# Performance work log

Hardware: AMD Instinct MI355X
Metric: run time of the kernel (lower is better)

## Reference

```python
import jax, jax.numpy as jnp
import numpy as np

B, DIM, HEADS, H, W, WS, AWS = 8, 64, 4, 256, 256, 8, 8
HD = DIM // HEADS
SCALE = HD ** -0.5


def _grid_sample_zeros(img, grid):
    # img: (N, C, Hi, Wi); grid: (N, Ho, Wo, 2) with (x, y) in [-1, 1]
    # bilinear, align_corners=True, zero padding (matches F.grid_sample)
    N, C, Hi, Wi = img.shape
    gx = (grid[..., 0] + 1.0) * 0.5 * (Wi - 1)
    gy = (grid[..., 1] + 1.0) * 0.5 * (Hi - 1)
    x0 = jnp.floor(gx).astype(jnp.int32); x1 = x0 + 1
    y0 = jnp.floor(gy).astype(jnp.int32); y1 = y0 + 1
    wx1 = gx - x0; wx0 = 1.0 - wx1
    wy1 = gy - y0; wy0 = 1.0 - wy1

    def one(im, x0, x1, y0, y1, wx0, wx1, wy0, wy1):
        def g(yi, xi):
            valid = ((yi >= 0) & (yi < Hi) & (xi >= 0) & (xi < Wi)).astype(im.dtype)
            v = im[:, jnp.clip(yi, 0, Hi - 1), jnp.clip(xi, 0, Wi - 1)]
            return v * valid[None]
        return (g(y0, x0) * (wy0 * wx0)[None] + g(y0, x1) * (wy0 * wx1)[None]
                + g(y1, x0) * (wy1 * wx0)[None] + g(y1, x1) * (wy1 * wx1)[None])

    return jax.vmap(one)(img, x0, x1, y0, y1, wx0, wx1, wy0, wy1)


def _rel_index():
    c = np.stack(np.meshgrid(np.arange(AWS), np.arange(AWS), indexing='ij'))
    cf = c.reshape(2, -1)
    rel = (cf[:, :, None] - cf[:, None, :]).transpose(1, 2, 0).copy()
    rel[:, :, 0] += AWS - 1
    rel[:, :, 1] += AWS - 1
    rel[:, :, 0] *= 2 * AWS - 1
    return rel.sum(-1)  # (AWS*AWS, AWS*AWS)


_REL_IDX = jnp.asarray(_rel_index())


def setup_inputs():
    key = jax.random.key(0)
    ks = jax.random.split(key, 8)
    s = 0.02
    return {
        'x': jax.random.normal(ks[0], (B, DIM, H, W), jnp.float32),
        'qkv_w': jax.random.normal(ks[1], (3 * DIM, DIM), jnp.float32) * s,
        'qkv_b': jnp.zeros((3 * DIM,), jnp.float32),
        'proj_w': jax.random.normal(ks[2], (DIM, DIM), jnp.float32) * s,
        'proj_b': jnp.zeros((DIM,), jnp.float32),
        'off_w': jax.random.normal(ks[3], (2 * HEADS, DIM), jnp.float32) * s,
        'off_b': jnp.zeros((2 * HEADS,), jnp.float32),
        'sc_w': jax.random.normal(ks[4], (2 * HEADS, DIM), jnp.float32) * s,
        'sc_b': jnp.zeros((2 * HEADS,), jnp.float32),
        'rel_bias': jax.random.normal(ks[5], ((WS + AWS - 1) ** 2, HEADS), jnp.float32) * s,
    }


def reference(x, qkv_w, qkv_b, proj_w, proj_b, off_w, off_b, sc_w, sc_b, rel_bias):
    b, dim, h, w = x.shape
    pad_td = (WS - h % WS) % WS; pad_lr = (WS - w % WS) % WS
    pt, pd = pad_td // 2, pad_td - pad_td // 2
    pl, pr = pad_lr // 2, pad_lr - pad_lr // 2
    eh, ew = h + pad_td, w + pad_lr
    wnh, wnw = eh // WS, ew // WS

    # per-pixel reference grid in [-1,1]; channel 0 = x(w-axis), channel 1 = y(h-axis)
    ref_h = jnp.linspace(-1.0, 1.0, eh)
    ref_w = jnp.linspace(-1.0, 1.0, ew)
    base = jnp.stack([jnp.broadcast_to(ref_w[None, :], (eh, ew)),
                      jnp.broadcast_to(ref_h[:, None], (eh, ew))], 0)
    base = base.reshape(2, wnh, WS, wnw, WS)

    # zero-mean window-relative attention coordinates
    bch = jnp.arange(AWS, dtype=jnp.float32) * 2 * WS / AWS / (eh - 1); bch = bch - bch.mean()
    bcw = jnp.arange(AWS, dtype=jnp.float32) * 2 * WS / AWS / (ew - 1); bcw = bcw - bcw.mean()
    ech = jnp.tile(bch, wnh)
    ecw = jnp.tile(bcw, wnw)
    wc = jnp.stack([jnp.broadcast_to(ecw[None, :], (wnh * AWS, wnw * AWS)),
                    jnp.broadcast_to(ech[:, None], (wnh * AWS, wnw * AWS))], 0)
    wc = wc.reshape(2, wnh, AWS, wnw, AWS)

    xp = jnp.pad(x, ((0, 0), (0, 0), (pt, pd), (pl, pr)))

    # offsets / scales: avgpool(WS) -> leaky_relu -> 1x1 conv
    pooled = xp.reshape(b, dim, wnh, WS, wnw, WS).mean(axis=(3, 5))
    act = jax.nn.leaky_relu(pooled, 0.01)
    off = jnp.einsum('bchw,oc->bohw', act, off_w) + off_b[None, :, None, None]
    off = off.reshape(b * HEADS, 2, wnh, wnw)
    off = off * jnp.array([1.0 / (h // WS), 1.0 / (w // WS)], off.dtype)[None, :, None, None]
    sc = jnp.einsum('bchw,oc->bohw', act, sc_w) + sc_b[None, :, None, None]
    sc = sc.reshape(b * HEADS, 2, wnh, wnw)

    coords = (base[None] + wc[None] * sc[:, :, :, None, :, None]
              + off[:, :, :, None, :, None])  # (b*heads, 2, wnh, AWS, wnw, AWS)
    grid = coords.transpose(0, 2, 3, 4, 5, 1).reshape(b * HEADS, wnh * AWS, wnw * AWS, 2)

    # qkv 1x1 conv, then spatial pad
    qkv = jnp.einsum('bchw,oc->bohw', x, qkv_w) + qkv_b[None, :, None, None]
    qkv = qkv.reshape(b, 3, HEADS, HD, h, w)
    qkv = jnp.pad(qkv, ((0, 0),) * 4 + ((pt, pd), (pl, pr)))
    q = qkv[:, 0].reshape(b * HEADS, HD, eh, ew)
    k = qkv[:, 1].reshape(b * HEADS, HD, eh, ew)
    v = qkv[:, 2].reshape(b * HEADS, HD, eh, ew)

    k_sel = _grid_sample_zeros(k, grid)
    v_sel = _grid_sample_zeros(v, grid)

    q = q.reshape(b, HEADS, HD, wnh, WS, wnw, WS).transpose(0, 3, 5, 1, 4, 6, 2)
    q = q.reshape(b * wnh * wnw, HEADS, WS * WS, HD)

    def to_win(t):
        t = t.reshape(b, HEADS, HD, wnh, AWS, wnw, AWS).transpose(0, 3, 5, 1, 4, 6, 2)
        return t.reshape(b * wnh * wnw, HEADS, AWS * AWS, HD)

    kw, vw = to_win(k_sel), to_win(v_sel)

    dots = jnp.einsum('wnqd,wnkd->wnqk', q, kw) * SCALE
    bias = rel_bias[_REL_IDX]  # (WS*WS, AWS*AWS, HEADS)
    dots = dots + bias.transpose(2, 0, 1)[None]
    attn = jax.nn.softmax(dots, axis=-1)
    out = jnp.einsum('wnqk,wnkd->wnqd', attn, vw)

    out = out.reshape(b, wnh, wnw, HEADS, WS, WS, HD).transpose(0, 3, 6, 1, 4, 2, 5)
    out = out.reshape(b, dim, eh, ew)[:, :, pt:h + pt, pl:w + pl]
    out = jnp.einsum('bchw,oc->bohw', out, proj_w) + proj_b[None, :, None, None]
    return out
```

## Files before the change

### kernel.cpp

```cpp
#include <hip/hip_runtime.h>

#define BATCH 8
#define CDIM 64
#define NHEADS 4
#define HD 16
#define IMG 256
#define WSZ 8
#define WN 32
#define NWIN (WN * WN)

static constexpr size_t OFFSC_FLOATS = (size_t)BATCH * NHEADS * NWIN * 4;
static constexpr size_t MAP_ELEMS = (size_t)BATCH * NHEADS * IMG * IMG * HD;

typedef unsigned short u16;
typedef __attribute__((ext_vector_type(2))) _Float16 h2;
typedef __attribute__((ext_vector_type(8))) _Float16 h8;
typedef __attribute__((ext_vector_type(4))) float f32x4;

__device__ __forceinline__ unsigned cvt_pk_f16(float a, float b) {
    unsigned r;
    asm("v_cvt_pkrtz_f16_f32 %0, %1, %2" : "=v"(r) : "v"(a), "v"(b));
    return r;
}
__device__ __forceinline__ float rcpf(float s) {
    float r;
    asm("v_rcp_f32 %0, %1" : "=v"(r) : "v"(s));
    return r;
}
union UH2 { unsigned u; h2 h; };
__device__ __forceinline__ h2 u2h2(unsigned u) { UH2 x; x.u = u; return x.h; }
__device__ __forceinline__ unsigned h22u(h2 h) { UH2 x; x.h = h; return x.u; }
__device__ __forceinline__ u16 f2h(float f) {
    _Float16 h = (_Float16)f;
    u16 r;
    __builtin_memcpy(&r, &h, 2);
    return r;
}
__device__ __forceinline__ unsigned pk_rne(float a, float b) {
    return (unsigned)f2h(a) | ((unsigned)f2h(b) << 16);
}

__global__ __launch_bounds__(256) void k_pool(const float* __restrict__ x,
                                              float* __restrict__ actg) {
    __shared__ float red[8][8][33];
    int bid = blockIdx.x;
    int cg = bid & 7, wh = (bid >> 3) & 31, b = bid >> 8;
    int t = threadIdx.x;
    int row = t >> 5, colg = t & 31;

    const float* xb = x + (((size_t)(b * CDIM + cg * 8) * IMG) + (size_t)(wh * WSZ + row)) * IMG + colg * 8;
    #pragma unroll
    for (int c = 0; c < 8; c++) {
        const float4* p4 = (const float4*)(xb + (size_t)c * IMG * IMG);
        float4 a = p4[0], bq = p4[1];
        red[c][row][colg] = a.x + a.y + a.z + a.w + bq.x + bq.y + bq.z + bq.w;
    }
    __syncthreads();
    int c = t >> 5, ww = t & 31;
    float s = 0.f;
    #pragma unroll
    for (int r = 0; r < 8; r++) s += red[c][r][ww];
    s *= (1.0f / 64.0f);
    s = (s >= 0.f) ? s : 0.01f * s;
    actg[(((size_t)b * CDIM + cg * 8 + c) * WN + wh) * WN + ww] = s;
}

__global__ __launch_bounds__(256) void k_offmv(const float* __restrict__ actg,
                                               const float* __restrict__ off_w,
                                               const float* __restrict__ off_b,
                                               const float* __restrict__ sc_w,
                                               const float* __restrict__ sc_b,
                                               float* __restrict__ offsc) {
    __shared__ float act[CDIM][WN + 1];
    int b = blockIdx.x >> 5, wh = blockIdx.x & 31;
    int t = threadIdx.x;
    for (int i = t; i < CDIM * WN; i += 256) {
        int c = i >> 5, ww = i & 31;
        act[c][ww] = actg[(((size_t)b * CDIM + c) * WN + wh) * WN + ww];
    }
    __syncthreads();
    int ww = t >> 3, oi = t & 7;
    float ao = off_b[oi], as = sc_b[oi];
    #pragma unroll 8
    for (int c = 0; c < CDIM; c++) {
        float av = act[c][ww];
        ao += av * off_w[oi * CDIM + c];
        as += av * sc_w[oi * CDIM + c];
    }
    ao *= (1.0f / 32.0f);
    int n = oi >> 1, d = oi & 1;
    size_t base = (((size_t)(b * NHEADS + n) * NWIN) + wh * WN + ww) << 2;
    offsc[base + d] = ao;
    offsc[base + 2 + d] = as;
}

__global__ __launch_bounds__(256) void k_wconv(const float* __restrict__ qkv_w,
                                               const float* __restrict__ proj_w,
                                               unsigned* __restrict__ wbf) {
    int i = blockIdx.x * 256 + threadIdx.x;
    if (i < 6144) {
        wbf[i] = cvt_pk_f16(qkv_w[2 * i], qkv_w[2 * i + 1]);
    } else if (i < 8192) {
        int j = i - 6144;
        wbf[i] = cvt_pk_f16(proj_w[2 * j], proj_w[2 * j + 1]);
    }
}

__global__ __launch_bounds__(256) void k_qkv_mfma(const float* __restrict__ x,
                                                  const u16* __restrict__ wbf,
                                                  const float* __restrict__ qkv_b,
                                                  u16* __restrict__ qm,
                                                  u16* __restrict__ km,
                                                  u16* __restrict__ vm) {
    __shared__ u16 Alds[256 * 64];

    int bid = blockIdx.x;
    bid = (bid & 7) * 256 + (bid >> 3);
    int b = bid >> 8, y = bid & 255;
    int t = threadIdx.x;

    {
        const float* xp = x + ((size_t)b * CDIM * IMG + y) * IMG + t;
        u16* row = Alds + t * 64;
        int sw = t & 7;
        #pragma unroll
        for (int cp = 0; cp < 32; cp++) {
            float a = xp[(size_t)(2 * cp) * IMG * IMG];
            float bq = xp[(size_t)(2 * cp + 1) * IMG * IMG];
            unsigned pk = cvt_pk_f16(a, bq);
            int c = 2 * cp;
            int chunk = c >> 3;
            *(unsigned*)(row + ((chunk ^ sw) << 3) + (c & 7)) = pk;
        }
    }

    int wv = t >> 6, l = t & 63;
    int lr = l & 15, lg = l >> 4;

    h8 afr[4][2];
    #pragma unroll
    for (int pg = 0; pg < 4; pg++) {
        int p = wv * 64 + pg * 16 + lr;
        const u16* prow = Alds + p * 64;
        int psw = p & 7;
        #pragma unroll
        for (int kb = 0; kb < 2; kb++) {
            int chunk = kb * 4 + lg;
            afr[pg][kb] = *(const h8*)(prow + ((chunk ^ psw) << 3));
        }
    }

    u16* const maps[3] = { qm, km, vm };
    #pragma unroll
    for (int ot = 0; ot < 12; ot++) {
        int o = ot * 16 + lr;
        float4 b4 = *(const float4*)(qkv_b + ot * 16 + lg * 4);
        h8 bfr0 = *(const h8*)(wbf + o * 64 + lg * 8);
        h8 bfr1 = *(const h8*)(wbf + o * 64 + 32 + lg * 8);

        f32x4 acc[4];
        #pragma unroll
        for (int pg = 0; pg < 4; pg++) {
            acc[pg] = (f32x4){ b4.x, b4.y, b4.z, b4.w };
            acc[pg] = __builtin_amdgcn_mfma_f32_16x16x32_f16(bfr0, afr[pg][0], acc[pg], 0, 0, 0);
            acc[pg] = __builtin_amdgcn_mfma_f32_16x16x32_f16(bfr1, afr[pg][1], acc[pg], 0, 0, 0);
        }

        u16* mp = maps[ot >> 2];
        int n = ot & 3;
        size_t base = ((size_t)(b * NHEADS + n) * IMG * IMG + (size_t)y * IMG) * HD;
        #pragma unroll
        for (int pg = 0; pg < 4; pg++) {
            size_t sb = base + (size_t)(wv * 64 + pg * 16 + lr) * HD + lg * 4;
            *(uint2*)(mp + sb) = make_uint2(pk_rne(acc[pg][0], acc[pg][1]),
                                            pk_rne(acc[pg][2], acc[pg][3]));
        }
    }
}

__global__ __launch_bounds__(256, 2) void k_attn3(const u16* __restrict__ qm,
                                                  const u16* __restrict__ km,
                                                  const u16* __restrict__ vm,
                                                  const u16* __restrict__ wproj,
                                                  const float* __restrict__ proj_b,
                                                  const float* __restrict__ rel_bias,
                                                  const float* __restrict__ offsc,
                                                  float* __restrict__ out) {
    __shared__ float biasS[NHEADS * 225];
    __shared__ _Float16 hb[NHEADS][2048];
    _Float16* Ob = &hb[0][0];

    int blk = blockIdx.x;
    blk = (blk & 7) * 1024 + (blk >> 3);
    int b = blk >> 10, wh = (blk >> 5) & 31, ww = blk & 31;
    int tid = threadIdx.x, n = tid >> 6, l = tid & 63;
    int g = l >> 4, cl = l & 15;
    int y0 = wh * WSZ, x0 = ww * WSZ;
    const h8 z8 = {};

    for (int i = tid; i < NHEADS * 225; i += 256) {
        int hn = i / 225, idx = i - hn * 225;
        biasS[i] = rel_bias[idx * NHEADS + hn] * 4.0f;
    }

    float4 os4 = *(const float4*)(offsc + ((((size_t)(b * NHEADS + n) * NWIN) + wh * WN + ww) << 2));

    h8 qfr[4];
    {
        const u16* qb = qm + ((size_t)(b * NHEADS + n) << 16) * HD;
        #pragma unroll
        for (int qt = 0; qt < 4; qt++) {
            int q = qt * 16 + cl;
            qfr[qt] = (g < 2)
                ? *(const h8*)(qb + ((size_t)(y0 + (q >> 3)) * IMG + (x0 + (q & 7))) * HD + g * 8)
                : z8;
        }
    }

    h8 wfr[2];
    #pragma unroll
    for (int h = 0; h < 2; h++)
        wfr[h] = *(const h8*)(wproj + (n * 16 + cl) * 64 + h * 32 + g * 8);
    float4 pb4 = *(const float4*)(proj_b + n * 16 + g * 4);

    {
        float offx = os4.x, offy = os4.y;
        float scx = os4.z, scy = os4.w;
        int pi = l >> 3, pj = l & 7;
        float gx = (float)(x0 + pj) + ((float)(2 * pj - 7) * (1.0f / 255.0f) * scx + offx) * 127.5f;
        float gy = (float)(y0 + pi) + ((float)(2 * pi - 7) * (1.0f / 255.0f) * scy + offy) * 127.5f;

        float fx0 = floorf(gx), fy0 = floorf(gy);
        int ix0 = (int)fx0, iy0 = (int)fy0;
        float wx1 = gx - fx0, wx0 = 1.f - wx1;
        float wy1 = gy - fy0, wy0 = 1.f - wy1;

        const u16* kb = km + ((size_t)(b * NHEADS + n) << 16) * HD;
        const u16* vb = vm + ((size_t)(b * NHEADS + n) << 16) * HD;

        int iys[2] = { iy0, iy0 + 1 };
        int ixs[2] = { ix0, ix0 + 1 };
        float wys[2] = { wy0, wy1 };
        float wxs[2] = { wx0, wx1 };

        size_t offs[4];
        h2 w2[4];
        #pragma unroll
        for (int t = 0; t < 4; t++) {
            int yy = iys[t >> 1], xq = ixs[t & 1];
            float wgt = wys[t >> 1] * wxs[t & 1];
            if (yy < 0 || yy >= IMG || xq < 0 || xq >= IMG) wgt = 0.f;
            int yc = min(max(yy, 0), IMG - 1), xc = min(max(xq, 0), IMG - 1);
            offs[t] = ((size_t)yc * IMG + xc) * HD;
            _Float16 hw = (_Float16)wgt;
            w2[t] = (h2){ hw, hw };
        }

        h2 kacc[8], vacc[8];
        #pragma unroll
        for (int i = 0; i < 8; i++) {
            kacc[i] = (h2){ (_Float16)0, (_Float16)0 };
            vacc[i] = (h2){ (_Float16)0, (_Float16)0 };
        }

        {
            uint4 t0[4], t1[4];
            #pragma unroll
            for (int t = 0; t < 4; t++) {
                const uint4* p = (const uint4*)(kb + offs[t]);
                t0[t] = p[0]; t1[t] = p[1];
            }
            #pragma unroll
            for (int t = 0; t < 4; t++) {
                kacc[0] += w2[t] * u2h2(t0[t].x); kacc[1] += w2[t] * u2h2(t0[t].y);
                kacc[2] += w2[t] * u2h2(t0[t].z); kacc[3] += w2[t] * u2h2(t0[t].w);
                kacc[4] += w2[t] * u2h2(t1[t].x); kacc[5] += w2[t] * u2h2(t1[t].y);
                kacc[6] += w2[t] * u2h2(t1[t].z); kacc[7] += w2[t] * u2h2(t1[t].w);
            }
        }
        {
            uint4 t0[4], t1[4];
            #pragma unroll
            for (int t = 0; t < 4; t++) {
                const uint4* p = (const uint4*)(vb + offs[t]);
                t0[t] = p[0]; t1[t] = p[1];
            }
            #pragma unroll
            for (int t = 0; t < 4; t++) {
                vacc[0] += w2[t] * u2h2(t0[t].x); vacc[1] += w2[t] * u2h2(t0[t].y);
                vacc[2] += w2[t] * u2h2(t0[t].z); vacc[3] += w2[t] * u2h2(t0[t].w);
                vacc[4] += w2[t] * u2h2(t1[t].x); vacc[5] += w2[t] * u2h2(t1[t].y);
                vacc[6] += w2[t] * u2h2(t1[t].z); vacc[7] += w2[t] * u2h2(t1[t].w);
            }
        }

        uint4* kp = (uint4*)(&hb[n][0] + (size_t)l * 16);
        kp[0] = make_uint4(h22u(kacc[0]), h22u(kacc[1]), h22u(kacc[2]), h22u(kacc[3]));
        kp[1] = make_uint4(h22u(kacc[4]), h22u(kacc[5]), h22u(kacc[6]), h22u(kacc[7]));

        int p = cl * 4 + g;
        #pragma unroll
        for (int i = 0; i < 8; i++) {
            int d0 = 2 * i, d1 = 2 * i + 1;
            hb[n][1024 + d0 * 64 + (p ^ ((d0 & 3) << 4))] = vacc[i][0];
            hb[n][1024 + d1 * 64 + (p ^ ((d1 & 3) << 4))] = vacc[i][1];
        }
    }

    h8 kfr[4], vfr[2];
    #pragma unroll
    for (int kt = 0; kt < 4; kt++)
        kfr[kt] = (g < 2) ? *(const h8*)(&hb[n][0] + (kt * 16 + cl) * 16 + g * 8) : z8;
    #pragma unroll
    for (int h = 0; h < 2; h++)
        vfr[h] = *(const h8*)(&hb[n][1024] + cl * 64 + ((h * 32 + g * 8) ^ ((cl & 3) << 4)));

    __syncthreads();

    f32x4 dacc[4][4];
    #pragma unroll
    for (int qt = 0; qt < 4; qt++) {
        #pragma unroll
        for (int kt = 0; kt < 4; kt++) {
            int pik = kt * 2 + (cl >> 3), pjk = cl & 7;
            int bidx = n * 225 + (7 - pik) * 15 + (7 - pjk) + (qt * 2 + (g >> 1)) * 15 + (g & 1) * 4;
            f32x4 c = { biasS[bidx], biasS[bidx + 1], biasS[bidx + 2], biasS[bidx + 3] };
            dacc[qt][kt] = __builtin_amdgcn_mfma_f32_16x16x32_f16(qfr[qt], kfr[kt], c, 0, 0, 0);
        }
    }

    _Float16* Pb = &hb[n][0];
    f32x4 oacc[4];
    float inv_[4][4];
    #pragma unroll
    for (int qt = 0; qt < 4; qt++) {
        #pragma unroll
        for (int kt = 0; kt < 4; kt++)
            #pragma unroll
            for (int r = 0; r < 4; r++)
                dacc[qt][kt][r] = exp2f(dacc[qt][kt][r] * 0.36067376f);
        #pragma unroll
        for (int r = 0; r < 4; r++) {
            float s0 = dacc[qt][0][r] + dacc[qt][1][r] + dacc[qt][2][r] + dacc[qt][3][r];
            #pragma unroll
            for (int s = 1; s < 16; s <<= 1) s0 += __shfl_xor(s0, s, 64);
            inv_[qt][r] = rcpf(s0);
        }
        #pragma unroll
        for (int r = 0; r < 4; r++) {
            unsigned lo = cvt_pk_f16(dacc[qt][0][r], dacc[qt][1][r]);
            unsigned hi = cvt_pk_f16(dacc[qt][2][r], dacc[qt][3][r]);
            *(uint2*)((u16*)Pb + (g * 4 + r) * 64 + ((cl * 4) ^ (r << 4))) = make_uint2(lo, hi);
        }
        f32x4 pv = { 0.f, 0.f, 0.f, 0.f };
        #pragma unroll
        for (int h = 0; h < 2; h++) {
            h8 af = *(const h8*)(Pb + cl * 64 + ((h * 32 + g * 8) ^ ((cl & 3) << 4)));
            pv = __builtin_amdgcn_mfma_f32_16x16x32_f16(af, vfr[h], pv, 0, 0, 0);
        }
        oacc[qt] = pv;
    }

    __syncthreads();

    #pragma unroll
    for (int qt = 0; qt < 4; qt++)
        #pragma unroll
        for (int r = 0; r < 4; r++) {
            int q = qt * 16 + g * 4 + r;
            Ob[q * 64 + ((n * 16 + cl) ^ (g << 4))] = (_Float16)(oacc[qt][r] * inv_[qt][r]);
        }
    __syncthreads();

    #pragma unroll
    for (int qt = 0; qt < 4; qt++) {
        f32x4 pa = { pb4.x, pb4.y, pb4.z, pb4.w };
        #pragma unroll
        for (int h = 0; h < 2; h++) {
            h8 of = *(const h8*)(Ob + (qt * 16 + cl) * 64 + ((h * 32 + g * 8) ^ ((cl >> 2) << 4)));
            pa = __builtin_amdgcn_mfma_f32_16x16x32_f16(wfr[h], of, pa, 0, 0, 0);
        }
        int q = qt * 16 + cl;
        #pragma unroll
        for (int r = 0; r < 4; r++) {
            out[((size_t)(b * CDIM + n * 16 + g * 4 + r) * IMG + y0 + (q >> 3)) * IMG + x0 + (q & 7)] = pa[r];
        }
    }
}

extern "C" void kernel_launch(void* const* d_in, const int* in_sizes, int n_in,
                              void* d_out, int out_size, void* d_ws, size_t ws_size,
                              hipStream_t stream) {
    const float* x      = (const float*)d_in[0];
    const float* qkv_w  = (const float*)d_in[1];
    const float* qkv_b  = (const float*)d_in[2];
    const float* proj_w = (const float*)d_in[3];
    const float* proj_b = (const float*)d_in[4];
    const float* off_w  = (const float*)d_in[5];
    const float* off_b  = (const float*)d_in[6];
    const float* sc_w   = (const float*)d_in[7];
    const float* sc_b   = (const float*)d_in[8];
    const float* rel_b  = (const float*)d_in[9];
    float* out = (float*)d_out;

    float* ws = (float*)d_ws;
    float* offsc = ws;
    u16* wqkv = (u16*)(ws + OFFSC_FLOATS);
    u16* wprj = wqkv + 12288;
    u16* qmm = wprj + 4096;
    u16* kmm = qmm + MAP_ELEMS;
    u16* vmm = kmm + MAP_ELEMS;
    float* actg = (float*)qmm;

    k_pool<<<BATCH * WN * 8, 256, 0, stream>>>(x, actg);
    k_offmv<<<BATCH * WN, 256, 0, stream>>>(actg, off_w, off_b, sc_w, sc_b, offsc);
    k_wconv<<<32, 256, 0, stream>>>(qkv_w, proj_w, (unsigned*)wqkv);
    k_qkv_mfma<<<BATCH * IMG, 256, 0, stream>>>(x, wqkv, qkv_b, qmm, kmm, vmm);
    k_attn3<<<BATCH * NWIN, 256, 0, stream>>>(qmm, kmm, vmm, wprj, proj_b,
                                              rel_b, offsc, out);
}
```

Before: 230.3 us.

## Fuse window average pooling into QKV kernel via shuffle-reduce and atomics

Removes the separate pooling kernel, which re-read the whole input, and folds the 8x8 window sum into the QKV projection kernel. Each thread group reduces its 8 columns with wave shuffles, and a lead lane atomically adds the partial sum into a zeroed buffer placed in the output tensor. The scale and leaky-ReLU move into the offset kernel. This saves a full pass over x but adds shuffles and many global float atomics inside the QKV load loop, plus a memset and a reordering of the kernels.

```diff
diff --git a/kernel.cpp b/kernel.cpp
--- a/kernel.cpp
+++ b/kernel.cpp
@@ -11,6 +11,7 @@
 
 static constexpr size_t OFFSC_FLOATS = (size_t)BATCH * NHEADS * NWIN * 4;
 static constexpr size_t MAP_ELEMS = (size_t)BATCH * NHEADS * IMG * IMG * HD;
+static constexpr size_t ACTG_BYTES = (size_t)BATCH * CDIM * WN * WN * 4;
 
 typedef unsigned short u16;
 typedef __attribute__((ext_vector_type(2))) _Float16 h2;
@@ -38,31 +39,6 @@
 }
 __device__ __forceinline__ unsigned pk_rne(float a, float b) {
     return (unsigned)f2h(a) | ((unsigned)f2h(b) << 16);
-}
-
-__global__ __launch_bounds__(256) void k_pool(const float* __restrict__ x,
-                                              float* __restrict__ actg) {
-    __shared__ float red[8][8][33];
-    int bid = blockIdx.x;
-    int cg = bid & 7, wh = (bid >> 3) & 31, b = bid >> 8;
-    int t = threadIdx.x;
-    int row = t >> 5, colg = t & 31;
-
-    const float* xb = x + (((size_t)(b * CDIM + cg * 8) * IMG) + (size_t)(wh * WSZ + row)) * IMG + colg * 8;
-    #pragma unroll
-    for (int c = 0; c < 8; c++) {
-        const float4* p4 = (const float4*)(xb + (size_t)c * IMG * IMG);
-        float4 a = p4[0], bq = p4[1];
-        red[c][row][colg] = a.x + a.y + a.z + a.w + bq.x + bq.y + bq.z + bq.w;
-    }
-    __syncthreads();
-    int c = t >> 5, ww = t & 31;
-    float s = 0.f;
-    #pragma unroll
-    for (int r = 0; r < 8; r++) s += red[c][r][ww];
-    s *= (1.0f / 64.0f);
-    s = (s >= 0.f) ? s : 0.01f * s;
-    actg[(((size_t)b * CDIM + cg * 8 + c) * WN + wh) * WN + ww] = s;
 }
 
 __global__ __launch_bounds__(256) void k_offmv(const float* __restrict__ actg,
@@ -76,7 +52,8 @@
     int t = threadIdx.x;
     for (int i = t; i < CDIM * WN; i += 256) {
         int c = i >> 5, ww = i & 31;
-        act[c][ww] = actg[(((size_t)b * CDIM + c) * WN + wh) * WN + ww];
+        float v = actg[(((size_t)b * CDIM + c) * WN + wh) * WN + ww] * (1.0f / 64.0f);
+        act[c][ww] = (v >= 0.f) ? v : 0.01f * v;
     }
     __syncthreads();
     int ww = t >> 3, oi = t & 7;
@@ -111,7 +88,8 @@
                                                   const float* __restrict__ qkv_b,
                                                   u16* __restrict__ qm,
                                                   u16* __restrict__ km,
-                                                  u16* __restrict__ vm) {
+                                                  u16* __restrict__ vm,
+                                                  float* __restrict__ actg) {
     __shared__ u16 Alds[256 * 64];
 
     int bid = blockIdx.x;
@@ -123,10 +101,23 @@
         const float* xp = x + ((size_t)b * CDIM * IMG + y) * IMG + t;
         u16* row = Alds + t * 64;
         int sw = t & 7;
+        int wh = y >> 3, ww = t >> 3;
+        float* ap = actg + (((size_t)b * CDIM) * WN + wh) * WN + ww;
+        bool lead = (t & 7) == 0;
         #pragma unroll
         for (int cp = 0; cp < 32; cp++) {
             float a = xp[(size_t)(2 * cp) * IMG * IMG];
             float bq = xp[(size_t)(2 * cp + 1) * IMG * IMG];
+            float sa = a, sb = bq;
+            #pragma unroll
+            for (int s = 1; s < 8; s <<= 1) {
+                sa += __shfl_xor(sa, s, 64);
+                sb += __shfl_xor(sb, s, 64);
+            }
+            if (lead) {
+                atomicAdd(ap + (size_t)(2 * cp) * (WN * WN), sa);
+                atomicAdd(ap + (size_t)(2 * cp + 1) * (WN * WN), sb);
+            }
             unsigned pk = cvt_pk_f16(a, bq);
             int c = 2 * cp;
             int chunk = c >> 3;
@@ -410,12 +401,12 @@
     u16* qmm = wprj + 4096;
     u16* kmm = qmm + MAP_ELEMS;
     u16* vmm = kmm + MAP_ELEMS;
-    float* actg = (float*)qmm;
-
-    k_pool<<<BATCH * WN * 8, 256, 0, stream>>>(x, actg);
+    float* actg = out;
+
+    hipMemsetAsync(actg, 0, ACTG_BYTES, stream);
+    k_wconv<<<32, 256, 0, stream>>>(qkv_w, proj_w, (unsigned*)wqkv);
+    k_qkv_mfma<<<BATCH * IMG, 256, 0, stream>>>(x, wqkv, qkv_b, qmm, kmm, vmm, actg);
     k_offmv<<<BATCH * WN, 256, 0, stream>>>(actg, off_w, off_b, sc_w, sc_b, offsc);
-    k_wconv<<<32, 256, 0, stream>>>(qkv_w, proj_w, (unsigned*)wqkv);
-    k_qkv_mfma<<<BATCH * IMG, 256, 0, stream>>>(x, wqkv, qkv_b, qmm, kmm, vmm);
     k_attn3<<<BATCH * NWIN, 256, 0, stream>>>(qmm, kmm, vmm, wprj, proj_b,
                                               rel_b, offsc, out);
 }
```

After: 234.1 us. About the same (+1.7%).
